# Kernel optimization log

Hardware: AMD Instinct MI355X
Metric: run time of the kernel (lower is better)

Reference implementation:

```python
import jax, jax.numpy as jnp
import numpy as np

N, E = 50000, 800000
IN, HID, HEADS, OUT = 128, 32, 8, 40
D1 = HID * HEADS  # 256


def setup_inputs() -> dict:
    key = jax.random.key(0)
    ks = jax.random.split(key, 24)

    def w(k, fin, fout):
        return (jax.random.normal(k, (fin, fout), jnp.float32) / np.sqrt(fin)).astype(jnp.float32)

    def b(k, fout):
        return (jax.random.normal(k, (fout,), jnp.float32) * 0.02).astype(jnp.float32)

    inp = {
        "x": jax.random.normal(ks[0], (N, IN), jnp.float32),
        "edge_index": jax.random.randint(ks[1], (2, E), 0, N, dtype=jnp.int64),
        # layer 1: TransformerConv(IN -> HID, heads=HEADS, concat=True, beta=True)
        "q1w": w(ks[2], IN, D1), "q1b": b(ks[3], D1),
        "k1w": w(ks[4], IN, D1), "k1b": b(ks[5], D1),
        "v1w": w(ks[6], IN, D1), "v1b": b(ks[7], D1),
        "s1w": w(ks[8], IN, D1), "s1b": b(ks[9], D1),
        "b1w": w(ks[10], 3 * D1, 1),
        # layer 2: TransformerConv(D1 -> OUT, heads=1, concat=False, beta=True)
        "q2w": w(ks[11], D1, OUT), "q2b": b(ks[12], OUT),
        "k2w": w(ks[13], D1, OUT), "k2b": b(ks[14], OUT),
        "v2w": w(ks[15], D1, OUT), "v2b": b(ks[16], OUT),
        "s2w": w(ks[17], D1, OUT), "s2b": b(ks[18], OUT),
        "b2w": w(ks[19], 3 * OUT, 1),
    }
    return inp


def _tconv(x, src, dst, qw, qb, kw, kb, vw, vb, sw, sb, bw, heads, ch, concat):
    """PyG TransformerConv (no edge_attr, root_weight=True, beta=True), eval mode."""
    n = x.shape[0]
    q = (x @ qw + qb).reshape(n, heads, ch)
    k = (x @ kw + kb).reshape(n, heads, ch)
    v = (x @ vw + vb).reshape(n, heads, ch)
    # per-edge attention logits: message flows src(j) -> dst(i)
    alpha = jnp.einsum("ehc,ehc->eh", q[dst], k[src]) / np.sqrt(ch)  # [E,H]
    # segment softmax over incoming edges of each dst node
    amax = jax.ops.segment_max(alpha, dst, num_segments=n)  # [N,H]
    a = jnp.exp(alpha - amax[dst])
    asum = jax.ops.segment_sum(a, dst, num_segments=n)  # [N,H]
    attn = a / asum[dst]  # [E,H]
    # scatter-aggregate weighted values
    out = jax.ops.segment_sum(v[src] * attn[:, :, None], dst, num_segments=n)  # [N,H,C]
    out = out.reshape(n, heads * ch) if concat else out.mean(axis=1)
    skip = x @ sw + sb
    beta = jax.nn.sigmoid(jnp.concatenate([out, skip, out - skip], axis=-1) @ bw)  # [N,1]
    return beta * skip + (1.0 - beta) * out


def reference(x, edge_index, q1w, q1b, k1w, k1b, v1w, v1b, s1w, s1b, b1w,
              q2w, q2b, k2w, k2b, v2w, v2b, s2w, s2b, b2w):
    src, dst = edge_index[0], edge_index[1]
    h = jax.nn.elu(_tconv(x, src, dst, q1w, q1b, k1w, k1b, v1w, v1b, s1w, s1b, b1w, HEADS, HID, True))
    return _tconv(h, src, dst, q2w, q2b, k2w, k2b, v2w, v2b, s2w, s2b, b2w, 1, OUT, False)
```

## Files before the change

kernel.cpp:

```cpp
#include <hip/hip_runtime.h>
#include <cstdint>
#include <cstddef>

#define N_NODES 50000
#define N_EDGES 800000
#define IN_F    128
#define HID     32
#define HEADS   8
#define OUT_F   40
#define D1      256
#define W1COLS  1024
#define W2COLS  160
#define CAP     64
#define CAPS    48

#define GFILL_B   3125
#define G1_BX     391
#define G1_BY     8
#define G1_GEMM_B (G1_BX * G1_BY)
#define G1_TOTAL  (GFILL_B + G1_GEMM_B)

typedef unsigned short ushortT;
typedef unsigned char  ucharT;
typedef unsigned long long ullT;
typedef unsigned short ushortx8 __attribute__((ext_vector_type(8)));
typedef __bf16 bf16x8 __attribute__((ext_vector_type(8)));
typedef float floatx4 __attribute__((ext_vector_type(4)));
typedef float floatx2 __attribute__((ext_vector_type(2)));

__device__ inline ushortT f2bf(float f) {
    union { float f; unsigned int u; } c; c.f = f;
    unsigned int r = c.u + 0x7FFFu + ((c.u >> 16) & 1u);
    return (ushortT)(r >> 16);
}
__device__ inline float bf2f(ushortT h) {
    union { unsigned int u; float f; } c; c.u = ((unsigned int)h) << 16; return c.f;
}

__device__ inline void g2lds16(const void* gptr, void* lptr) {
    __builtin_amdgcn_global_load_lds(
        (const __attribute__((address_space(1))) unsigned int*)gptr,
        (__attribute__((address_space(3))) unsigned int*)lptr,
        16, 0, 0);
}

#define PREP_CONV_B  6250
#define PREP_W1_B    512
#define PREP_W2_B    160
#define PREP_TOTAL_B (PREP_CONV_B + PREP_W1_B + PREP_W2_B)

__global__ __launch_bounds__(256) void k_prep(
        const float* __restrict__ x, ushortT* __restrict__ xb,
        const float* __restrict__ q1w, const float* __restrict__ k1w,
        const float* __restrict__ v1w, const float* __restrict__ s1w,
        const float* __restrict__ q1b, const float* __restrict__ k1b,
        const float* __restrict__ v1b, const float* __restrict__ s1b,
        ushortT* __restrict__ W1T, float* __restrict__ b1c,
        const float* __restrict__ q2w, const float* __restrict__ k2w,
        const float* __restrict__ v2w, const float* __restrict__ s2w,
        const float* __restrict__ q2b, const float* __restrict__ k2b,
        const float* __restrict__ v2b, const float* __restrict__ s2b,
        ushortT* __restrict__ W2T, float* __restrict__ b2c) {
    int b = blockIdx.x;
    int tid = threadIdx.x;
    if (b < PREP_CONV_B) {
        int i = b * 256 + tid;
        float4 v = reinterpret_cast<const float4*>(x)[i];
        ushort4 o;
        o.x = f2bf(v.x); o.y = f2bf(v.y); o.z = f2bf(v.z); o.w = f2bf(v.w);
        reinterpret_cast<ushort4*>(xb)[i] = o;
    } else if (b < PREP_CONV_B + PREP_W1_B) {
        int t = (b - PREP_CONV_B) * 256 + tid;
        int c = t / IN_F, k = t % IN_F;
        int sel = c >> 8, cc = c & 255;
        const float* w = sel == 0 ? q1w : sel == 1 ? k1w : sel == 2 ? v1w : s1w;
        W1T[(size_t)c * IN_F + k] = f2bf(w[(size_t)k * D1 + cc]);
        if (k == 0) {
            const float* bb = sel == 0 ? q1b : sel == 1 ? k1b : sel == 2 ? v1b : s1b;
            b1c[c] = bb[cc];
        }
    } else {
        int t = (b - PREP_CONV_B - PREP_W1_B) * 256 + tid;
        int c = t / D1, k = t % D1;
        int sel = c / OUT_F, cc = c % OUT_F;
        const float* w = sel == 0 ? q2w : sel == 1 ? k2w : sel == 2 ? v2w : s2w;
        W2T[(size_t)c * D1 + k] = f2bf(w[(size_t)k * OUT_F + cc]);
        if (k == 0) {
            const float* bb = sel == 0 ? q2b : sel == 1 ? k2b : sel == 2 ? v2b : s2b;
            b2c[c] = bb[cc];
        }
    }
}

template<int MODE>
__global__ __launch_bounds__(256) void gemm_mfma_pack(
        const ushortT* __restrict__ A, const ushortT* __restrict__ BT,
        const float* __restrict__ bias, float* __restrict__ QSf,
        ushortT* __restrict__ QSh, ucharT* __restrict__ KV8,
        ushortT* __restrict__ K2V2,
        const int* __restrict__ ei, int* __restrict__ cursor, int* __restrict__ col,
        int M, int K, int Nn) {
    constexpr int TM = 128, TN = 128, TK = 32;
    __shared__ float smemf[8192];
    int bx2, by2;
    if (MODE == 1) {
        int t = blockIdx.x;
        int idx;
        bool isFill;
        if (t < 2 * GFILL_B) { isFill = !(t & 1); idx = t >> 1; }
        else                 { isFill = false;    idx = t - GFILL_B; }
        if (isFill) {
            int e = idx * 256 + threadIdx.x;
            if (e < N_EDGES) {
                int dd = ei[N_EDGES + e];
                int p = atomicAdd(&cursor[dd], 1);
                col[dd * CAP + p] = ei[e];
            }
            return;
        }
        bx2 = idx / G1_BY;
        by2 = idx % G1_BY;
    } else {
        bx2 = blockIdx.x;
        by2 = blockIdx.y;
    }
    int tid = threadIdx.x;
    int lane = tid & 63, wave = tid >> 6;
    int bm = bx2 * TM, bn = by2 * TN;
    int wm = (wave & 1) * 64, wn = (wave >> 1) * 64;
    int mrow = lane & 15, g = lane >> 4;
    int wbase = tid & ~63;
    int rsA0 = min(bm + (tid >> 2), M - 1);
    int rsA1 = min(bm + ((256 + tid) >> 2), M - 1);
    int rsB0 = min(bn + (tid >> 2), Nn - 1);
    int rsB1 = min(bn + ((256 + tid) >> 2), Nn - 1);
    int cs = (tid & 3) * 8;
    const ushortT* pA0 = A + (size_t)rsA0 * K + cs;
    const ushortT* pA1 = A + (size_t)rsA1 * K + cs;
    const ushortT* pB0 = BT + (size_t)rsB0 * K + cs;
    const ushortT* pB1 = BT + (size_t)rsB1 * K + cs;

    int cb4 = (lane & 15) * 4;
    float4 bv = make_float4(0.f, 0.f, 0.f, 0.f);
    if (MODE == 1) bv = *reinterpret_cast<const float4*>(bias + by2 * 128 + wn + cb4);

    auto stage = [&](int sel, int k0) {
        char* base = (char*)smemf + sel * 16384;
        g2lds16(pA0 + k0, base + (size_t)wbase * 16);
        g2lds16(pA1 + k0, base + (size_t)(256 + wbase) * 16);
        g2lds16(pB0 + k0, base + 8192 + (size_t)wbase * 16);
        g2lds16(pB1 + k0, base + 8192 + (size_t)(256 + wbase) * 16);
    };

    int nt = K / TK;
    floatx4 acc[4][4] = {};
    stage(0, 0);
    for (int t = 0; t < nt; ++t) {
        if (t + 1 < nt) {
            stage((t + 1) & 1, (t + 1) * TK);
            __builtin_amdgcn_sched_barrier(0);
            asm volatile("s_waitcnt vmcnt(4)" ::: "memory");
        } else {
            __builtin_amdgcn_sched_barrier(0);
            asm volatile("s_waitcnt vmcnt(0)" ::: "memory");
        }
        __builtin_amdgcn_s_barrier();
        __builtin_amdgcn_sched_barrier(0);
        {
            const ushortT* As = (const ushortT*)((char*)smemf + (t & 1) * 16384);
            const ushortT* Bs = As + TM * TK;
            bf16x8 a[4], b[4];
#pragma unroll
            for (int i = 0; i < 4; ++i)
                a[i] = *reinterpret_cast<const bf16x8*>(As + (wm + i * 16 + mrow) * TK + g * 8);
#pragma unroll
            for (int j = 0; j < 4; ++j)
                b[j] = *reinterpret_cast<const bf16x8*>(Bs + (wn + j * 16 + mrow) * TK + g * 8);
#pragma unroll
            for (int i = 0; i < 4; ++i)
#pragma unroll
                for (int j = 0; j < 4; ++j)
                    acc[i][j] = __builtin_amdgcn_mfma_f32_16x16x32_bf16(a[i], b[j], acc[i][j], 0, 0, 0);
        }
        __builtin_amdgcn_sched_barrier(0);
        __builtin_amdgcn_s_barrier();
    }

    if (MODE == 1) {
        float* lds = smemf + wave * 1088;
        int sec = by2 >> 1;
        int ccbase = (by2 & 1) * 128 + wn;
        int rlo = lane >> 4;
#pragma unroll
        for (int i = 0; i < 4; ++i) {
#pragma unroll
            for (int j = 0; j < 4; ++j)
#pragma unroll
                for (int r = 0; r < 4; ++r)
                    lds[(g * 4 + r) * 68 + j * 16 + mrow] = acc[i][j][r];
#pragma unroll
            for (int it = 0; it < 4; ++it) {
                int row = it * 4 + rlo;
                int gm = bm + wm + i * 16 + row;
                if (gm >= M) continue;
                float4 v = *reinterpret_cast<float4*>(lds + row * 68 + cb4);
                v.x += bv.x; v.y += bv.y; v.z += bv.z; v.w += bv.w;
                int cc = ccbase + cb4;
                if (sec == 0 || sec == 3) {
                    ushort4 h;
                    h.x = f2bf(v.x); h.y = f2bf(v.y); h.z = f2bf(v.z); h.w = f2bf(v.w);
                    ushortT* dst = QSh + (size_t)gm * 512 + (sec == 3 ? 256 : 0) + cc;
                    *reinterpret_cast<ushort4*>(dst) = h;
                } else {
                    unsigned int pk = 0;
                    pk = __builtin_amdgcn_cvt_pk_fp8_f32(v.x, v.y, pk, false);
                    pk = __builtin_amdgcn_cvt_pk_fp8_f32(v.z, v.w, pk, true);
                    ucharT* dst = KV8 + (size_t)gm * 512 + (sec == 2 ? 256 : 0) + cc;
                    *reinterpret_cast<unsigned int*>(dst) = pk;
                }
            }
        }
    } else {
#pragma unroll
        for (int i = 0; i < 4; ++i) {
#pragma unroll
            for (int j = 0; j < 4; ++j) {
                int gn = bn + wn + j * 16 + mrow;
                if (gn >= Nn) continue;
                float bvs = bias[gn];
#pragma unroll
                for (int r = 0; r < 4; ++r) {
                    int gm = bm + wm + i * 16 + g * 4 + r;
                    if (gm >= M) continue;
                    float val = acc[i][j][r] + bvs;
                    int sec = gn / OUT_F, cc = gn % OUT_F;
                    if (sec == 0)      QSf[(size_t)gm * 80 + cc] = val;
                    else if (sec == 1) K2V2[(size_t)gm * 80 + cc] = f2bf(val);
                    else if (sec == 2) K2V2[(size_t)gm * 80 + 40 + cc] = f2bf(val);
                    else               QSf[(size_t)gm * 80 + 40 + cc] = val;
                }
            }
        }
    }
}

__global__ __launch_bounds__(256) void k_edge1(
        const ushortT* __restrict__ QSh, const ucharT* __restrict__ KV8,
        const float* __restrict__ bw,
        const int* __restrict__ degc, const int* __restrict__ col,
        ushortT* __restrict__ H1b) {
    int gid  = blockIdx.x * blockDim.x + threadIdx.x;
    int lane = threadIdx.x & 63;
    int node = __builtin_amdgcn_readfirstlane(gid >> 6);
    if (node >= N_NODES) return;
    const float scale = 0.17677669529663687f;
    bool isV = lane >= 32;
    ushortx8 qs8 = *reinterpret_cast<const ushortx8*>(QSh + (size_t)node * 512 + lane * 8);
    float qsc = isV ? 1.0f : scale;
    floatx2 q01, q23, q45, q67;
    q01[0] = bf2f(qs8[0]) * qsc; q01[1] = bf2f(qs8[1]) * qsc;
    q23[0] = bf2f(qs8[2]) * qsc; q23[1] = bf2f(qs8[3]) * qsc;
    q45[0] = bf2f(qs8[4]) * qsc; q45[1] = bf2f(qs8[5]) * qsc;
    q67[0] = bf2f(qs8[6]) * qsc; q67[1] = bf2f(qs8[7]) * qsc;

    float l = 0.f;
    floatx2 acc0 = {0.f, 0.f}, acc1 = {0.f, 0.f}, acc2 = {0.f, 0.f}, acc3 = {0.f, 0.f};
    const int* colp = col + node * CAP;
    int d = degc[node];
    int voff = lane * 8;

#define EDGE_BODY(kv) do {                                                              \
    floatx2 a0 = __builtin_amdgcn_cvt_pk_f32_fp8((unsigned)(kv), false);                \
    floatx2 a1 = __builtin_amdgcn_cvt_pk_f32_fp8((unsigned)(kv), true);                 \
    floatx2 a2 = __builtin_amdgcn_cvt_pk_f32_fp8((unsigned)((kv) >> 32), false);        \
    floatx2 a3 = __builtin_amdgcn_cvt_pk_f32_fp8((unsigned)((kv) >> 32), true);         \
    floatx2 pd = q01 * a0 + q23 * a1 + q45 * a2 + q67 * a3;                             \
    float p = pd[0] + pd[1];                                                            \
    p += __int_as_float(__builtin_amdgcn_update_dpp(                                    \
             0, __float_as_int(p), 0xB1, 0xF, 0xF, false));    \
    p += __int_as_float(__builtin_amdgcn_update_dpp(                                    \
             0, __float_as_int(p), 0x4E, 0xF, 0xF, false));    \
    float e = __expf(p);                                                                \
    float eb = __shfl(e, lane & 31);             \
    l += eb;                                                                            \
    floatx2 ev = {eb, eb};                                                              \
    acc0 += ev * a0; acc1 += ev * a1; acc2 += ev * a2; acc3 += ev * a3;                 \
} while (0)

    int t = 0;
    for (; t + 4 <= d; t += 4) {
        int4 js = *reinterpret_cast<const int4*>(colp + t);
        ullT kv0 = *reinterpret_cast<const ullT*>(KV8 + ((size_t)js.x << 9) + voff);
        ullT kv1 = *reinterpret_cast<const ullT*>(KV8 + ((size_t)js.y << 9) + voff);
        ullT kv2 = *reinterpret_cast<const ullT*>(KV8 + ((size_t)js.z << 9) + voff);
        ullT kv3 = *reinterpret_cast<const ullT*>(KV8 + ((size_t)js.w << 9) + voff);
        EDGE_BODY(kv0);
        EDGE_BODY(kv1);
        EDGE_BODY(kv2);
        EDGE_BODY(kv3);
    }
    for (; t < d; ++t) {
        int j = colp[t];
        ullT kv = *reinterpret_cast<const ullT*>(KV8 + ((size_t)j << 9) + voff);
        EDGE_BODY(kv);
    }
#undef EDGE_BODY

    float inv = (l > 0.f) ? 1.f / l : 0.f;
    floatx2 iv = {inv, inv};
    floatx2 o0 = acc0 * iv, o1 = acc1 * iv, o2 = acc2 * iv, o3 = acc3 * iv;
    int cb = isV ? (lane - 32) * 8 : 0;
    float4 wa0 = *reinterpret_cast<const float4*>(bw + cb);
    float4 wa1 = *reinterpret_cast<const float4*>(bw + cb + 4);
    float4 wb0 = *reinterpret_cast<const float4*>(bw + D1 + cb);
    float4 wb1 = *reinterpret_cast<const float4*>(bw + D1 + cb + 4);
    float4 wc0 = *reinterpret_cast<const float4*>(bw + 2 * D1 + cb);
    float4 wc1 = *reinterpret_cast<const float4*>(bw + 2 * D1 + cb + 4);
    float part = 0.f;
    if (isV) {
        part = o0[0] * wa0.x + o0[1] * wa0.y + o1[0] * wa0.z + o1[1] * wa0.w
             + o2[0] * wa1.x + o2[1] * wa1.y + o3[0] * wa1.z + o3[1] * wa1.w
             + q01[0] * wb0.x + q01[1] * wb0.y + q23[0] * wb0.z + q23[1] * wb0.w
             + q45[0] * wb1.x + q45[1] * wb1.y + q67[0] * wb1.z + q67[1] * wb1.w
             + (o0[0] - q01[0]) * wc0.x + (o0[1] - q01[1]) * wc0.y
             + (o1[0] - q23[0]) * wc0.z + (o1[1] - q23[1]) * wc0.w
             + (o2[0] - q45[0]) * wc1.x + (o2[1] - q45[1]) * wc1.y
             + (o3[0] - q67[0]) * wc1.z + (o3[1] - q67[1]) * wc1.w;
    }
#pragma unroll
    for (int s = 1; s < 32; s <<= 1) part += __shfl_xor(part, s);
    float beta = 1.f / (1.f + __expf(-part));
    if (isV) {
        float h[8];
        h[0] = beta * q01[0] + (1.f - beta) * o0[0];
        h[1] = beta * q01[1] + (1.f - beta) * o0[1];
        h[2] = beta * q23[0] + (1.f - beta) * o1[0];
        h[3] = beta * q23[1] + (1.f - beta) * o1[1];
        h[4] = beta * q45[0] + (1.f - beta) * o2[0];
        h[5] = beta * q45[1] + (1.f - beta) * o2[1];
        h[6] = beta * q67[0] + (1.f - beta) * o3[0];
        h[7] = beta * q67[1] + (1.f - beta) * o3[1];
        ushortx8 hb;
#pragma unroll
        for (int c = 0; c < 8; ++c) {
            float hv = h[c] > 0.f ? h[c] : __expf(h[c]) - 1.f;
            hb[c] = f2bf(hv);
        }
        *reinterpret_cast<ushortx8*>(H1b + (size_t)node * D1 + (lane - 32) * 8) = hb;
    }
}

__global__ __launch_bounds__(256) void k_edge2(
        const float* __restrict__ QS, const ushortT* __restrict__ K2V2,
        const float* __restrict__ bw,
        const int* __restrict__ degc, const int* __restrict__ col,
        float* __restrict__ out) {
    __shared__ float        qbuf[4][40];
    __shared__ unsigned int ksm[4][CAPS * 21];
    int gid  = blockIdx.x * blockDim.x + threadIdx.x;
    int node = gid >> 6;
    int wave = threadIdx.x >> 6;
    int lane = threadIdx.x & 63;
    if (node >= N_NODES) return;
    const float scale = 0.15811388300841897f;
    bool act = lane < OUT_F;
    if (act) qbuf[wave][lane] = QS[(size_t)node * 80 + lane] * scale;

    int d = degc[node];
    int jmine = (lane < d) ? col[node * CAP + lane] : 0;

    const unsigned int* Kdw = reinterpret_cast<const unsigned int*>(K2V2);
    int sr = lane / 20;
    int sc = lane - sr * 20;
    for (int r0 = 0; r0 < d; r0 += 3) {
        int rr = r0 + sr;
        int jrr = __shfl(jmine, rr);
        if (lane < 60 && rr < d)
            ksm[wave][rr * 21 + sc] = Kdw[(size_t)jrr * 40 + sc];
    }

    float p = 0.f;
    if (lane < d) {
        float s = 0.f;
#pragma unroll
        for (int c = 0; c < 20; ++c) {
            unsigned int kk = ksm[wave][lane * 21 + c];
            s += qbuf[wave][2 * c]     * bf2f((ushortT)(kk & 0xFFFFu))
               + qbuf[wave][2 * c + 1] * bf2f((ushortT)(kk >> 16));
        }
        p = __expf(s);
    }
    float l = p;
#pragma unroll
    for (int s = 1; s < 64; s <<= 1) l += __shfl_xor(l, s);

    float acc = 0.f;
    int ln = act ? lane : 0;
    int e = 0;
    for (; e + 8 <= d; e += 8) {
        float vv[8], aa[8];
#pragma unroll
        for (int u = 0; u < 8; ++u) {
            int je = __shfl(jmine, e + u);
            aa[u] = __shfl(p, e + u);
            vv[u] = bf2f(K2V2[(size_t)je * 80 + 40 + ln]);
        }
#pragma unroll
        for (int u = 0; u < 8; ++u) acc += aa[u] * vv[u];
    }
    if (e + 4 <= d) {
        float vv[4], aa[4];
#pragma unroll
        for (int u = 0; u < 4; ++u) {
            int je = __shfl(jmine, e + u);
            aa[u] = __shfl(p, e + u);
            vv[u] = bf2f(K2V2[(size_t)je * 80 + 40 + ln]);
        }
#pragma unroll
        for (int u = 0; u < 4; ++u) acc += aa[u] * vv[u];
        e += 4;
    }
    for (; e < d; ++e) {
        int je = __shfl(jmine, e);
        float ae = __shfl(p, e);
        acc += ae * bf2f(K2V2[(size_t)je * 80 + 40 + ln]);
    }

    float inv = (l > 0.f) ? 1.f / l : 0.f;
    float o  = acc * inv;
    float sk = act ? QS[(size_t)node * 80 + 40 + lane] : 0.f;
    float part = act ? (o * bw[lane] + sk * bw[OUT_F + lane] + (o - sk) * bw[2 * OUT_F + lane]) : 0.f;
#pragma unroll
    for (int s = 1; s < 64; s <<= 1) part += __shfl_xor(part, s);
    float beta = 1.f / (1.f + __expf(-part));
    if (act) out[(size_t)node * OUT_F + lane] = beta * sk + (1.f - beta) * o;
}

extern "C" void kernel_launch(void* const* d_in, const int* in_sizes, int n_in,
                              void* d_out, int out_size, void* d_ws, size_t ws_size,
                              hipStream_t stream) {
    const float* x   = (const float*)d_in[0];
    const int*   ei  = (const int*)d_in[1];
    const float* q1w = (const float*)d_in[2];
    const float* q1b = (const float*)d_in[3];
    const float* k1w = (const float*)d_in[4];
    const float* k1b = (const float*)d_in[5];
    const float* v1w = (const float*)d_in[6];
    const float* v1b = (const float*)d_in[7];
    const float* s1w = (const float*)d_in[8];
    const float* s1b = (const float*)d_in[9];
    const float* b1w = (const float*)d_in[10];
    const float* q2w = (const float*)d_in[11];
    const float* q2b = (const float*)d_in[12];
    const float* k2w = (const float*)d_in[13];
    const float* k2b = (const float*)d_in[14];
    const float* v2w = (const float*)d_in[15];
    const float* v2b = (const float*)d_in[16];
    const float* s2w = (const float*)d_in[17];
    const float* s2b = (const float*)d_in[18];
    const float* b2w = (const float*)d_in[19];
    float* out = (float*)d_out;

    char* w = (char*)d_ws;
    ushortT* QSh = (ushortT*)w;
    ucharT*  KV8 = (ucharT*)(w + 51200000);
    ushortT* H1b = (ushortT*)(w + 102400000);
    ushortT* xb  = (ushortT*)(w + 128000000);
    ushortT* W1T = (ushortT*)(w + 140800000);
    ushortT* W2T = (ushortT*)(w + 141062144);
    float*   b1c = (float*)(w + 141144064);
    float*   b2c = (float*)(w + 141148160);
    int* cursor  = (int*)(w + 141149184);
    int* col     = cursor + N_NODES;
    float*   QS2  = (float*)w;
    ushortT* K2V2 = (ushortT*)(w + 51200000);

    hipMemsetAsync(cursor, 0, N_NODES * sizeof(int), stream);

    k_prep<<<PREP_TOTAL_B, 256, 0, stream>>>(
        x, xb,
        q1w, k1w, v1w, s1w, q1b, k1b, v1b, s1b, W1T, b1c,
        q2w, k2w, v2w, s2w, q2b, k2b, v2b, s2b, W2T, b2c);

    gemm_mfma_pack<1><<<G1_TOTAL, 256, 0, stream>>>(
        xb, W1T, b1c, nullptr, QSh, KV8, nullptr,
        ei, cursor, col, N_NODES, IN_F, W1COLS);

    k_edge1<<<(N_NODES * 64) / 256, 256, 0, stream>>>(QSh, KV8, b1w, cursor, col, H1b);

    dim3 g2((N_NODES + 127) / 128, (W2COLS + 127) / 128);
    gemm_mfma_pack<2><<<g2, 256, 0, stream>>>(H1b, W2T, b2c, QS2, nullptr, nullptr,
                                              K2V2, nullptr, nullptr, nullptr,
                                              N_NODES, D1, W2COLS);

    k_edge2<<<(N_NODES * 64) / 256, 256, 0, stream>>>(QS2, K2V2, b2w, cursor, col, out);
}
```

Baseline: 308.2 us.

## Process two edges per wave in layer-1 edge kernel with 16-byte lanes

```diff
diff --git a/kernel.cpp b/kernel.cpp
--- a/kernel.cpp
+++ b/kernel.cpp
@@ -35,6 +35,14 @@
 }
 __device__ inline float bf2f(ushortT h) {
     union { unsigned int u; float f; } c; c.u = ((unsigned int)h) << 16; return c.f;
+}
+
+__device__ inline float ex2(float x) {
+#if __has_builtin(__builtin_amdgcn_exp2f)
+    return __builtin_amdgcn_exp2f(x);
+#else
+    return __expf(x * 0.6931471805599453f);
+#endif
 }
 
 __device__ inline void g2lds16(const void* gptr, void* lptr) {
@@ -253,100 +261,121 @@
     int lane = threadIdx.x & 63;
     int node = __builtin_amdgcn_readfirstlane(gid >> 6);
     if (node >= N_NODES) return;
-    const float scale = 0.17677669529663687f;
-    bool isV = lane >= 32;
-    ushortx8 qs8 = *reinterpret_cast<const ushortx8*>(QSh + (size_t)node * 512 + lane * 8);
-    float qsc = isV ? 1.0f : scale;
-    floatx2 q01, q23, q45, q67;
-    q01[0] = bf2f(qs8[0]) * qsc; q01[1] = bf2f(qs8[1]) * qsc;
-    q23[0] = bf2f(qs8[2]) * qsc; q23[1] = bf2f(qs8[3]) * qsc;
-    q45[0] = bf2f(qs8[4]) * qsc; q45[1] = bf2f(qs8[5]) * qsc;
-    q67[0] = bf2f(qs8[6]) * qsc; q67[1] = bf2f(qs8[7]) * qsc;
+    int s    = lane & 31;
+    int half = lane >> 5;
+    const float SCL = 0.17677669529663687f * 1.4426950408889634f;
+    float qsc = (s < 16) ? SCL : 1.0f;
+    const ushortT* qrow = QSh + (size_t)node * 512 + s * 16;
+    ushortx8 w0 = *reinterpret_cast<const ushortx8*>(qrow);
+    ushortx8 w1 = *reinterpret_cast<const ushortx8*>(qrow + 8);
+    floatx2 q[8];
+#pragma unroll
+    for (int i = 0; i < 4; ++i) {
+        q[i][0]     = bf2f(w0[2 * i])     * qsc;
+        q[i][1]     = bf2f(w0[2 * i + 1]) * qsc;
+        q[i + 4][0] = bf2f(w1[2 * i])     * qsc;
+        q[i + 4][1] = bf2f(w1[2 * i + 1]) * qsc;
+    }
 
     float l = 0.f;
-    floatx2 acc0 = {0.f, 0.f}, acc1 = {0.f, 0.f}, acc2 = {0.f, 0.f}, acc3 = {0.f, 0.f};
+    floatx2 acc[8] = {};
     const int* colp = col + node * CAP;
     int d = degc[node];
-    int voff = lane * 8;
-
-#define EDGE_BODY(kv) do {                                                              \
-    floatx2 a0 = __builtin_amdgcn_cvt_pk_f32_fp8((unsigned)(kv), false);                \
-    floatx2 a1 = __builtin_amdgcn_cvt_pk_f32_fp8((unsigned)(kv), true);                 \
-    floatx2 a2 = __builtin_amdgcn_cvt_pk_f32_fp8((unsigned)((kv) >> 32), false);        \
-    floatx2 a3 = __builtin_amdgcn_cvt_pk_f32_fp8((unsigned)((kv) >> 32), true);         \
-    floatx2 pd = q01 * a0 + q23 * a1 + q45 * a2 + q67 * a3;                             \
+    int boff = s * 16;
+    int bidx = (lane & 32) | ((s < 16) ? s : ((s - 16) & ~1));
+
+#define PAIR_BODY(kv, maskOdd) do {                                                     \
+    floatx2 a0 = __builtin_amdgcn_cvt_pk_f32_fp8((kv).x, false);                        \
+    floatx2 a1 = __builtin_amdgcn_cvt_pk_f32_fp8((kv).x, true);                         \
+    floatx2 a2 = __builtin_amdgcn_cvt_pk_f32_fp8((kv).y, false);                        \
+    floatx2 a3 = __builtin_amdgcn_cvt_pk_f32_fp8((kv).y, true);                         \
+    floatx2 a4 = __builtin_amdgcn_cvt_pk_f32_fp8((kv).z, false);                        \
+    floatx2 a5 = __builtin_amdgcn_cvt_pk_f32_fp8((kv).z, true);                         \
+    floatx2 a6 = __builtin_amdgcn_cvt_pk_f32_fp8((kv).w, false);                        \
+    floatx2 a7 = __builtin_amdgcn_cvt_pk_f32_fp8((kv).w, true);                         \
+    floatx2 pd = q[0] * a0 + q[1] * a1 + q[2] * a2 + q[3] * a3                          \
+               + q[4] * a4 + q[5] * a5 + q[6] * a6 + q[7] * a7;                         \
     float p = pd[0] + pd[1];                                                            \
     p += __int_as_float(__builtin_amdgcn_update_dpp(                                    \
              0, __float_as_int(p), 0xB1, 0xF, 0xF, false));    \
-    p += __int_as_float(__builtin_amdgcn_update_dpp(                                    \
-             0, __float_as_int(p), 0x4E, 0xF, 0xF, false));    \
-    float e = __expf(p);                                                                \
-    float eb = __shfl(e, lane & 31);             \
+    float e = ex2(p);                                                                   \
+    float eb = __shfl(e, bidx);                                                         \
+    if (maskOdd && half) eb = 0.f;                                                      \
     l += eb;                                                                            \
     floatx2 ev = {eb, eb};                                                              \
-    acc0 += ev * a0; acc1 += ev * a1; acc2 += ev * a2; acc3 += ev * a3;                 \
+    acc[0] += ev * a0; acc[1] += ev * a1; acc[2] += ev * a2; acc[3] += ev * a3;         \
+    acc[4] += ev * a4; acc[5] += ev * a5; acc[6] += ev * a6; acc[7] += ev * a7;         \
 } while (0)
 
     int t = 0;
     for (; t + 4 <= d; t += 4) {
         int4 js = *reinterpret_cast<const int4*>(colp + t);
-        ullT kv0 = *reinterpret_cast<const ullT*>(KV8 + ((size_t)js.x << 9) + voff);
-        ullT kv1 = *reinterpret_cast<const ullT*>(KV8 + ((size_t)js.y << 9) + voff);
-        ullT kv2 = *reinterpret_cast<const ullT*>(KV8 + ((size_t)js.z << 9) + voff);
-        ullT kv3 = *reinterpret_cast<const ullT*>(KV8 + ((size_t)js.w << 9) + voff);
-        EDGE_BODY(kv0);
-        EDGE_BODY(kv1);
-        EDGE_BODY(kv2);
-        EDGE_BODY(kv3);
-    }
-    for (; t < d; ++t) {
-        int j = colp[t];
-        ullT kv = *reinterpret_cast<const ullT*>(KV8 + ((size_t)j << 9) + voff);
-        EDGE_BODY(kv);
-    }
-#undef EDGE_BODY
-
+        int ja = half ? js.y : js.x;
+        int jb = half ? js.w : js.z;
+        uint4 kva = *reinterpret_cast<const uint4*>(KV8 + ((size_t)ja << 9) + boff);
+        uint4 kvb = *reinterpret_cast<const uint4*>(KV8 + ((size_t)jb << 9) + boff);
+        PAIR_BODY(kva, false);
+        PAIR_BODY(kvb, false);
+    }
+    if (t + 2 <= d) {
+        int2 js = *reinterpret_cast<const int2*>(colp + t);
+        int ja = half ? js.y : js.x;
+        uint4 kv = *reinterpret_cast<const uint4*>(KV8 + ((size_t)ja << 9) + boff);
+        PAIR_BODY(kv, false);
+        t += 2;
+    }
+    if (t < d) {
+        int ja = colp[t];
+        uint4 kv = *reinterpret_cast<const uint4*>(KV8 + ((size_t)ja << 9) + boff);
+        PAIR_BODY(kv, true);
+    }
+#undef PAIR_BODY
+
+#pragma unroll
+    for (int i = 0; i < 8; ++i) {
+        acc[i][0] += __shfl_xor(acc[i][0], 32);
+        acc[i][1] += __shfl_xor(acc[i][1], 32);
+    }
+    l += __shfl_xor(l, 32);
     float inv = (l > 0.f) ? 1.f / l : 0.f;
-    floatx2 iv = {inv, inv};
-    floatx2 o0 = acc0 * iv, o1 = acc1 * iv, o2 = acc2 * iv, o3 = acc3 * iv;
-    int cb = isV ? (lane - 32) * 8 : 0;
-    float4 wa0 = *reinterpret_cast<const float4*>(bw + cb);
-    float4 wa1 = *reinterpret_cast<const float4*>(bw + cb + 4);
-    float4 wb0 = *reinterpret_cast<const float4*>(bw + D1 + cb);
-    float4 wb1 = *reinterpret_cast<const float4*>(bw + D1 + cb + 4);
-    float4 wc0 = *reinterpret_cast<const float4*>(bw + 2 * D1 + cb);
-    float4 wc1 = *reinterpret_cast<const float4*>(bw + 2 * D1 + cb + 4);
+
     float part = 0.f;
-    if (isV) {
-        part = o0[0] * wa0.x + o0[1] * wa0.y + o1[0] * wa0.z + o1[1] * wa0.w
-             + o2[0] * wa1.x + o2[1] * wa1.y + o3[0] * wa1.z + o3[1] * wa1.w
-             + q01[0] * wb0.x + q01[1] * wb0.y + q23[0] * wb0.z + q23[1] * wb0.w
-             + q45[0] * wb1.x + q45[1] * wb1.y + q67[0] * wb1.z + q67[1] * wb1.w
-             + (o0[0] - q01[0]) * wc0.x + (o0[1] - q01[1]) * wc0.y
-             + (o1[0] - q23[0]) * wc0.z + (o1[1] - q23[1]) * wc0.w
-             + (o2[0] - q45[0]) * wc1.x + (o2[1] - q45[1]) * wc1.y
-             + (o3[0] - q67[0]) * wc1.z + (o3[1] - q67[1]) * wc1.w;
-    }
-#pragma unroll
-    for (int s = 1; s < 32; s <<= 1) part += __shfl_xor(part, s);
+    if (half == 0 && s >= 16) {
+        int cbb = (s - 16) * 16;
+#pragma unroll
+        for (int i2 = 0; i2 < 4; ++i2) {
+            float4 wA = *reinterpret_cast<const float4*>(bw + cbb + 4 * i2);
+            float4 wB = *reinterpret_cast<const float4*>(bw + D1 + cbb + 4 * i2);
+            float4 wC = *reinterpret_cast<const float4*>(bw + 2 * D1 + cbb + 4 * i2);
+            float oA = acc[2 * i2][0] * inv,     oB = acc[2 * i2][1] * inv;
+            float oC = acc[2 * i2 + 1][0] * inv, oD = acc[2 * i2 + 1][1] * inv;
+            float sA = q[2 * i2][0],     sB = q[2 * i2][1];
+            float sC = q[2 * i2 + 1][0], sD = q[2 * i2 + 1][1];
+            part += oA * wA.x + oB * wA.y + oC * wA.z + oD * wA.w
+                  + sA * wB.x + sB * wB.y + sC * wB.z + sD * wB.w
+                  + (oA - sA) * wC.x + (oB - sB) * wC.y
+                  + (oC - sC) * wC.z + (oD - sD) * wC.w;
+        }
+    }
+#pragma unroll
+    for (int sh = 1; sh < 64; sh <<= 1) part += __shfl_xor(part, sh);
     float beta = 1.f / (1.f + __expf(-part));
-    if (isV) {
-        float h[8];
-        h[0] = beta * q01[0] + (1.f - beta) * o0[0];
-        h[1] = beta * q01[1] + (1.f - beta) * o0[1];
-        h[2] = beta * q23[0] + (1.f - beta) * o1[0];
-        h[3] = beta * q23[1] + (1.f - beta) * o1[1];
-        h[4] = beta * q45[0] + (1.f - beta) * o2[0];
-        h[5] = beta * q45[1] + (1.f - beta) * o2[1];
-        h[6] = beta * q67[0] + (1.f - beta) * o3[0];
-        h[7] = beta * q67[1] + (1.f - beta) * o3[1];
+    if (s >= 16) {
+        int i0 = half * 4;
         ushortx8 hb;
 #pragma unroll
-        for (int c = 0; c < 8; ++c) {
-            float hv = h[c] > 0.f ? h[c] : __expf(h[c]) - 1.f;
-            hb[c] = f2bf(hv);
-        }
-        *reinterpret_cast<ushortx8*>(H1b + (size_t)node * D1 + (lane - 32) * 8) = hb;
+        for (int k = 0; k < 4; ++k) {
+            float o0 = acc[i0 + k][0] * inv, o1 = acc[i0 + k][1] * inv;
+            float s0 = q[i0 + k][0],         s1 = q[i0 + k][1];
+            float h0 = beta * s0 + (1.f - beta) * o0;
+            float h1 = beta * s1 + (1.f - beta) * o1;
+            h0 = h0 > 0.f ? h0 : __expf(h0) - 1.f;
+            h1 = h1 > 0.f ? h1 : __expf(h1) - 1.f;
+            hb[2 * k]     = f2bf(h0);
+            hb[2 * k + 1] = f2bf(h1);
+        }
+        *reinterpret_cast<ushortx8*>(
+            H1b + (size_t)node * D1 + (s - 16) * 16 + half * 8) = hb;
     }
 }
 
@@ -362,7 +391,7 @@
     int wave = threadIdx.x >> 6;
     int lane = threadIdx.x & 63;
     if (node >= N_NODES) return;
-    const float scale = 0.15811388300841897f;
+    const float scale = 0.15811388300841897f * 1.4426950408889634f;
     bool act = lane < OUT_F;
     if (act) qbuf[wave][lane] = QS[(size_t)node * 80 + lane] * scale;
 
@@ -381,14 +410,14 @@
 
     float p = 0.f;
     if (lane < d) {
-        float s = 0.f;
+        float sdot = 0.f;
 #pragma unroll
         for (int c = 0; c < 20; ++c) {
             unsigned int kk = ksm[wave][lane * 21 + c];
-            s += qbuf[wave][2 * c]     * bf2f((ushortT)(kk & 0xFFFFu))
-               + qbuf[wave][2 * c + 1] * bf2f((ushortT)(kk >> 16));
-        }
-        p = __expf(s);
+            sdot += qbuf[wave][2 * c]     * bf2f((ushortT)(kk & 0xFFFFu))
+                  + qbuf[wave][2 * c + 1] * bf2f((ushortT)(kk >> 16));
+        }
+        p = ex2(sdot);
     }
     float l = p;
 #pragma unroll
```

Measured after the change: 355.2 us. 15.2% more time.
